# Optimization experiments

Hardware: AMD Instinct MI355X
Metric: run time of the kernel (lower is better)

The kernel has to match this reference:

```python
import jax, jax.numpy as jnp
import numpy as np

B, S, H = 2, 1024, 2048
NH, NKV, HD = 32, 8, 64
EPS = 1e-6
ROPE_BASE = 10000.0


def rms_norm(x, w, eps=EPS):
    xf = x.astype(jnp.float32)
    var = jnp.mean(xf * xf, axis=-1, keepdims=True)
    return (w * (xf * jax.lax.rsqrt(var + eps))).astype(x.dtype)


def rotate_half(x):
    x1, x2 = jnp.split(x, 2, axis=-1)
    return jnp.concatenate((-x2, x1), axis=-1)


def setup_inputs() -> dict:
    key = jax.random.key(0)
    ks = jax.random.split(key, 8)
    hidden_states = jax.random.normal(ks[0], (B, S, H), dtype=jnp.float32) * 0.02
    # real rotary embeddings for positions 0..S-1
    inv_freq = 1.0 / (ROPE_BASE ** (jnp.arange(0, HD, 2, dtype=jnp.float32) / HD))
    freqs = jnp.arange(S, dtype=jnp.float32)[:, None] * inv_freq[None, :]  # [S, HD/2]
    emb = jnp.concatenate((freqs, freqs), axis=-1)  # [S, HD]
    cos = jnp.broadcast_to(jnp.cos(emb)[None], (B, S, HD)).astype(jnp.float32)
    sin = jnp.broadcast_to(jnp.sin(emb)[None], (B, S, HD)).astype(jnp.float32)
    # additive causal mask [B, 1, S, S]
    causal = jnp.tril(jnp.ones((S, S), dtype=bool))
    attention_mask = jnp.broadcast_to(
        jnp.where(causal, 0.0, -1e9).astype(jnp.float32)[None, None], (B, 1, S, S))
    scale_in = 1.0 / np.sqrt(H)
    wq = jax.random.normal(ks[1], (H, NH * HD), dtype=jnp.float32) * scale_in
    wk = jax.random.normal(ks[2], (H, NKV * HD), dtype=jnp.float32) * scale_in
    wv = jax.random.normal(ks[3], (H, NKV * HD), dtype=jnp.float32) * scale_in
    wo = jax.random.normal(ks[4], (NH * HD, H), dtype=jnp.float32) * scale_in
    q_norm_w = jnp.ones((NH * HD,), dtype=jnp.float32)
    k_norm_w = jnp.ones((NKV * HD,), dtype=jnp.float32)
    return {"hidden_states": hidden_states, "cos": cos, "sin": sin,
            "attention_mask": attention_mask, "wq": wq, "wk": wk, "wv": wv,
            "wo": wo, "q_norm_w": q_norm_w, "k_norm_w": k_norm_w}


def reference(hidden_states, cos, sin, attention_mask, wq, wk, wv, wo, q_norm_w, k_norm_w):
    b, s, _ = hidden_states.shape
    scaling = HD ** -0.5
    groups = NH // NKV
    # projections + QK-norm (RMSNorm over full projected dim, before head split)
    q = rms_norm(hidden_states @ wq, q_norm_w)
    k = rms_norm(hidden_states @ wk, k_norm_w)
    v = hidden_states @ wv
    q = q.reshape(b, s, NH, HD).transpose(0, 2, 1, 3)   # [b, nh, s, hd]
    k = k.reshape(b, s, NKV, HD).transpose(0, 2, 1, 3)  # [b, nkv, s, hd]
    v = v.reshape(b, s, NKV, HD).transpose(0, 2, 1, 3)
    # RoPE (cos/sin broadcast over head dim)
    c = cos[:, None]  # [b, 1, s, hd]
    sn = sin[:, None]
    q = q * c + rotate_half(q) * sn
    k = k * c + rotate_half(k) * sn
    # GQA: repeat KV heads
    k = jnp.repeat(k, groups, axis=1)  # [b, nh, s, hd]
    v = jnp.repeat(v, groups, axis=1)
    scores = jnp.einsum('bhqd,bhkd->bhqk', q, k) * scaling + attention_mask
    attn = jax.nn.softmax(scores.astype(jnp.float32), axis=-1).astype(q.dtype)
    out = jnp.einsum('bhqk,bhkd->bhqd', attn, v)
    out = out.transpose(0, 2, 1, 3).reshape(b, s, NH * HD)
    return out @ wo
```

## Files before the change

### kernel.cpp

```cpp
#include <hip/hip_runtime.h>

#define B_    2
#define S_    1024
#define NH_   32
#define NKV_  8
#define T_    (B_*S_)

typedef unsigned short u16;
typedef unsigned int u32;
typedef __attribute__((ext_vector_type(8))) short bf16x8;
typedef __attribute__((ext_vector_type(4))) float f32x4;

__device__ __forceinline__ float bf2f(u16 u) {
    union { float f; unsigned int i; } c; c.i = ((unsigned int)u) << 16; return c.f;
}
__device__ __forceinline__ u16 f2bf(float f) {
    union { float f; unsigned int u; } c; c.f = f;
    return (u16)((c.u + 0x7FFFu + ((c.u >> 16) & 1u)) >> 16);
}

__device__ __forceinline__ void gld_lds16(const void* g, void* s) {
    __builtin_amdgcn_global_load_lds(
        (const __attribute__((address_space(1))) void*)g,
        (__attribute__((address_space(3))) void*)s,
        16, 0, 0);
}

__global__ __launch_bounds__(256) void preproc1(
    const float* __restrict__ hidden, const float* __restrict__ wq,
    const float* __restrict__ wk, const float* __restrict__ wv,
    const float* __restrict__ wo,
    u16* __restrict__ hidden_bf, u16* __restrict__ wqkvT, u16* __restrict__ woT)
{
    __shared__ float t[64][65];
    const int bid = blockIdx.x, tid = threadIdx.x;
    if (bid < 2048) {
        int i = (bid * 256 + tid) * 8;
        float4 v0 = *reinterpret_cast<const float4*>(&hidden[i]);
        float4 v1 = *reinterpret_cast<const float4*>(&hidden[i + 4]);
        u16 o[8] = { f2bf(v0.x), f2bf(v0.y), f2bf(v0.z), f2bf(v0.w),
                     f2bf(v1.x), f2bf(v1.y), f2bf(v1.z), f2bf(v1.w) };
        *reinterpret_cast<uint4*>(&hidden_bf[i]) = *reinterpret_cast<uint4*>(o);
        return;
    }
    const float* src; int scol, sN, n0, k0;
    u16* dst; int dK;
    if (bid < 3584) {
        const int tt = bid - 2048;
        n0 = (tt % 48) * 64; k0 = (tt / 48) * 64;
        if (n0 < 2048)      { src = wq; scol = n0;        sN = 2048; }
        else if (n0 < 2560) { src = wk; scol = n0 - 2048; sN = 512;  }
        else                { src = wv; scol = n0 - 2560; sN = 512;  }
        dst = wqkvT; dK = 2048;
    } else {
        const int tt = bid - 3584;
        n0 = (tt % 32) * 64; k0 = (tt / 32) * 64;
        src = wo; scol = n0; sN = 2048;
        dst = woT; dK = 2048;
    }
    #pragma unroll
    for (int i = 0; i < 16; ++i) {
        int e = i * 256 + tid, r = e >> 6, c = e & 63;
        t[r][c] = src[(size_t)(k0 + r) * sN + scol + c];
    }
    __syncthreads();
    #pragma unroll
    for (int i = 0; i < 16; ++i) {
        int e = i * 256 + tid, rr = e >> 6, cc = e & 63;
        dst[(size_t)(n0 + rr) * dK + k0 + cc] = f2bf(t[cc][rr]);
    }
}

template<bool OUT_BF16>
__global__ __launch_bounds__(256) void gemm_bt(
    const u16* __restrict__ A, const u16* __restrict__ Bt,
    void* __restrict__ Cv, int M, int N, int K)
{
    __shared__ u16 As[2][128 * 64];
    __shared__ u16 Bs[2][64 * 64];
    const int MB = M >> 7;
    const int cpx = gridDim.x >> 3;
    const int L = (blockIdx.x & 7) * cpx + (blockIdx.x >> 3);
    const int bm = (L % MB) * 128, bn = (L / MB) * 64;
    const int tid = threadIdx.x;
    const int w = tid >> 6, lane = tid & 63;
    const int wr = w >> 1, wc = w & 1;
    const int l15 = lane & 15, lg = lane >> 4;
    const int srow = lane >> 3;
    const int scolsw = (lane & 7) ^ srow;

    f32x4 acc[4][2] = {};
    const int nk = K >> 6;

#define GSTAGE(ks, bb) do {                                                    \
    const int kofs = (ks) * 64;                                                \
    _Pragma("unroll")                                                          \
    for (int i_ = 0; i_ < 4; ++i_) {                                           \
        int chunk_ = w * 4 + i_;                                               \
        int row_ = chunk_ * 8 + srow;                                          \
        gld_lds16(&A[(size_t)(bm + row_) * K + kofs + scolsw * 8],             \
                  &As[bb][chunk_ * 512]);                                      \
    }                                                                          \
    _Pragma("unroll")                                                          \
    for (int j_ = 0; j_ < 2; ++j_) {                                           \
        int chunk_ = w * 2 + j_;                                               \
        int row_ = chunk_ * 8 + srow;                                          \
        gld_lds16(&Bt[(size_t)(bn + row_) * K + kofs + scolsw * 8],            \
                  &Bs[bb][chunk_ * 512]);                                      \
    } } while (0)

    GSTAGE(0, 0);
    for (int ks = 0; ks < nk; ++ks) {
        const int cur = ks & 1;
        if (ks + 1 < nk) {
            GSTAGE(ks + 1, cur ^ 1);
            asm volatile("s_waitcnt vmcnt(6)" ::: "memory");
        } else {
            asm volatile("s_waitcnt vmcnt(0)" ::: "memory");
        }
        __builtin_amdgcn_sched_barrier(0);
        __builtin_amdgcn_s_barrier();
        __builtin_amdgcn_sched_barrier(0);

        #pragma unroll
        for (int kk = 0; kk < 2; ++kk) {
            const int phys = ((kk * 4 + lg) ^ (l15 & 7)) * 8;
            bf16x8 a[4], b[2];
            #pragma unroll
            for (int m = 0; m < 4; ++m)
                a[m] = *reinterpret_cast<const bf16x8*>(
                    &As[cur][(wr * 64 + m * 16 + l15) * 64 + phys]);
            #pragma unroll
            for (int n = 0; n < 2; ++n)
                b[n] = *reinterpret_cast<const bf16x8*>(
                    &Bs[cur][(wc * 32 + n * 16 + l15) * 64 + phys]);
            #pragma unroll
            for (int m = 0; m < 4; ++m)
                #pragma unroll
                for (int n = 0; n < 2; ++n)
                    acc[m][n] = __builtin_amdgcn_mfma_f32_16x16x32_bf16(
                        a[m], b[n], acc[m][n], 0, 0, 0);
        }
        __builtin_amdgcn_sched_barrier(0);
        __builtin_amdgcn_s_barrier();
    }
#undef GSTAGE

    const int orow0 = bm + wr * 64, ocol0 = bn + wc * 32;
    #pragma unroll
    for (int m = 0; m < 4; ++m)
        #pragma unroll
        for (int n = 0; n < 2; ++n)
            #pragma unroll
            for (int r = 0; r < 4; ++r) {
                int row = orow0 + m * 16 + lg * 4 + r;
                int col = ocol0 + n * 16 + l15;
                float v = acc[m][n][r];
                if (OUT_BF16)
                    ((u16*)Cv)[(size_t)row * N + col] = f2bf(v);
                else
                    ((float*)Cv)[(size_t)row * N + col] = v;
            }
}

template<int DIM>
__device__ __forceinline__ void rms_rope_row(
    u16* base, const float* __restrict__ w,
    const float* __restrict__ cs, const float* __restrict__ sn,
    float* row, float* red, int tid)
{
    float ss = 0.f;
    for (int i0 = tid * 8; i0 < DIM; i0 += 2048) {
        uint4 u = *reinterpret_cast<const uint4*>(&base[i0]);
        const u16* us = reinterpret_cast<const u16*>(&u);
        #pragma unroll
        for (int j = 0; j < 8; ++j) { float f = bf2f(us[j]); row[i0 + j] = f; ss += f * f; }
    }
    #pragma unroll
    for (int off = 1; off < 64; off <<= 1) ss += __shfl_xor(ss, off);
    if ((tid & 63) == 0) red[tid >> 6] = ss;
    __syncthreads();
    const float rstd = rsqrtf((red[0] + red[1] + red[2] + red[3]) * (1.0f / DIM) + 1e-6f);

    for (int i0 = tid * 8; i0 < DIM; i0 += 2048) {
        u16 o[8];
        #pragma unroll
        for (int j = 0; j < 8; ++j) {
            int i = i0 + j, dh = i & 63, bb = i & ~63;
            int oi = (dh < 32) ? bb + dh + 32 : bb + dh - 32;
            float y     = row[i]  * rstd * w[i];
            float other = row[oi] * rstd * w[oi];
            if (dh < 32) other = -other;
            o[j] = f2bf(y * cs[dh] + other * sn[dh]);
        }
        *reinterpret_cast<uint4*>(&base[i0]) = *reinterpret_cast<uint4*>(o);
    }
}

__global__ __launch_bounds__(256) void rmsnorm_rope_vt(
    u16* __restrict__ x, const float* __restrict__ qnw, const float* __restrict__ knw,
    const float* __restrict__ cosb, const float* __restrict__ sinb,
    u16* __restrict__ vT)
{
    __shared__ float smem[2304];
    const int bid = blockIdx.x, tid = threadIdx.x;
    if (bid < 2048) {
        const int t = bid;
        float* row = smem;
        float* red = smem + 2048;
        const float* cs = cosb + (size_t)t * 64;
        const float* sn = sinb + (size_t)t * 64;
        rms_rope_row<2048>(x + (size_t)t * 3072,        qnw, cs, sn, row, red, tid);
        __syncthreads();
        rms_rope_row<512 >(x + (size_t)t * 3072 + 2048, knw, cs, sn, row, red, tid);
        return;
    }
    u16 (*tu)[72] = reinterpret_cast<u16(*)[72]>(smem);
    const int bid2 = bid - 2048;
    const int hd = bid2 % 16;
    const int s0 = (bid2 / 16) * 64;
    const int b = hd >> 3, kvh = hd & 7;
    #pragma unroll
    for (int i = 0; i < 2; ++i) {
        int chunk = i * 256 + tid;
        int r = chunk >> 3, c8 = (chunk & 7) * 8;
        uint4 u = *reinterpret_cast<const uint4*>(
            &x[(size_t)(b * 1024 + s0 + r) * 3072 + 2560 + kvh * 64 + c8]);
        *reinterpret_cast<uint4*>(&tu[r][c8]) = u;
    }
    __syncthreads();
    #pragma unroll
    for (int i = 0; i < 2; ++i) {
        int chunk = i * 256 + tid;
        int d = chunk >> 3, c8 = (chunk & 7) * 8;
        u16 o[8];
        #pragma unroll
        for (int j = 0; j < 8; ++j) o[j] = tu[c8 + j][d];
        *reinterpret_cast<uint4*>(&vT[((size_t)(hd * 64 + d)) * 1024 + s0 + c8])
            = *reinterpret_cast<uint4*>(o);
    }
}

__global__ __launch_bounds__(256) void attn_pair(
    const u16* __restrict__ qkv,
    const u16* __restrict__ vT,
    u16* __restrict__ ob)
{
    __shared__ u16 Ks[2][64 * 64];
    __shared__ u16 Vs[2][64 * 64];
    __shared__ u16 Ps[4][16 * 64];

    const int bid = blockIdx.x;
    const int L   = (bid & 7) * 64 + (bid >> 3);
    const int g5  = L >> 5;
    const int rem = L & 31;
    const int ha  = rem & 3;
    const int p   = rem >> 2;
    const int b = g5 >> 3, kvh = g5 & 7;
    const int h = kvh * 4 + ha;
    const int qtA = p, qtB = 15 - p;

    const int tid = threadIdx.x, w = tid >> 6, lane = tid & 63;
    const int l15 = lane & 15, lg = lane >> 4;
    const int srow = lane >> 3;
    const int scolsw = (lane & 7) ^ srow;

    bf16x8 qfA[2], qfB[2];
    {
        const size_t rA = (size_t)(b * 1024 + qtA * 64 + w * 16 + l15);
        const size_t rB = (size_t)(b * 1024 + qtB * 64 + w * 16 + l15);
        #pragma unroll
        for (int kk = 0; kk < 2; ++kk) {
            qfA[kk] = *reinterpret_cast<const bf16x8*>(
                &qkv[rA * 3072 + h * 64 + kk * 32 + lg * 8]);
            qfB[kk] = *reinterpret_cast<const bf16x8*>(
                &qkv[rB * 3072 + h * 64 + kk * 32 + lg * 8]);
        }
    }
    asm volatile("s_waitcnt vmcnt(0)" ::: "memory");

    float lrA = 0.f, lrB = 0.f;
    f32x4 oaccA[4] = {}, oaccB[4] = {};

    const u16* kbase = qkv + 2048 + kvh * 64;
    const u16* vbase = vT + (size_t)(g5 * 64) * 1024;
    const int qgA = qtA * 64 + w * 16 + l15;
    const int qgB = qtB * 64 + w * 16 + l15;

#define ASTAGE(kt, bb) do {                                                    \
    _Pragma("unroll")                                                          \
    for (int i_ = 0; i_ < 2; ++i_) {                                           \
        int chunk_ = w * 2 + i_;                                               \
        int row_ = chunk_ * 8 + srow;                                          \
        gld_lds16(&kbase[(size_t)(b * 1024 + (kt) * 64 + row_) * 3072          \
                         + scolsw * 8], &Ks[bb][chunk_ * 512]);                \
        gld_lds16(&vbase[(size_t)row_ * 1024 + (kt) * 64 + scolsw * 8],        \
                  &Vs[bb][chunk_ * 512]);                                      \
    } } while (0)

    auto step = [&](int kt, int cur, const bf16x8 (&qf)[2],
                    float& lr, f32x4 (&oacc)[4], int qg, bool dz) {
        f32x4 sacc[4] = {};
        #pragma unroll
        for (int kk = 0; kk < 2; ++kk) {
            const int phys = ((kk * 4 + lg) ^ (l15 & 7)) * 8;
            #pragma unroll
            for (int m = 0; m < 4; ++m) {
                bf16x8 kf = *reinterpret_cast<const bf16x8*>(
                    &Ks[cur][(m * 16 + l15) * 64 + phys]);
                sacc[m] = __builtin_amdgcn_mfma_f32_16x16x32_bf16(
                    kf, qf[kk], sacc[m], 0, 0, 0);
            }
        }

        float ls = 0.f;
        #pragma unroll
        for (int m = 0; m < 4; ++m) {
            u16 pk[4];
            #pragma unroll
            for (int r = 0; r < 4; ++r) {
                float v = sacc[m][r] * 0.18033688f;
                if (dz && (kt * 64 + m * 16 + lg * 4 + r > qg)) v = -1e30f;
                float e = exp2f(v);
                ls += e;
                pk[r] = f2bf(e);
            }
            const int keyc = m * 16 + lg * 4;
            const int phys = (keyc >> 3) ^ (l15 & 7);
            *reinterpret_cast<uint2*>(&Ps[w][l15 * 64 + phys * 8 + (keyc & 7)])
                = *reinterpret_cast<const uint2*>(pk);
        }
        lr += ls;

        asm volatile("s_waitcnt lgkmcnt(0)" ::: "memory");
        __builtin_amdgcn_sched_barrier(0);

        #pragma unroll
        for (int kk = 0; kk < 2; ++kk) {
            const int phys = ((kk * 4 + lg) ^ (l15 & 7)) * 8;
            bf16x8 pf = *reinterpret_cast<const bf16x8*>(
                &Ps[w][l15 * 64 + phys]);
            #pragma unroll
            for (int d = 0; d < 4; ++d) {
                bf16x8 vf = *reinterpret_cast<const bf16x8*>(
                    &Vs[cur][(d * 16 + l15) * 64 + phys]);
                oacc[d] = __builtin_amdgcn_mfma_f32_16x16x32_bf16(
                    pf, vf, oacc[d], 0, 0, 0);
            }
        }
    };

    ASTAGE(0, 0);
    for (int s = 0; s <= 16; ++s) {
        const int cur = s & 1;
        if (s < 16) {
            const int ktn = (s + 1 <= p) ? (s + 1) : (s - p);
            ASTAGE(ktn, cur ^ 1);
            asm volatile("s_waitcnt vmcnt(4)" ::: "memory");
        } else {
            asm volatile("s_waitcnt vmcnt(0)" ::: "memory");
        }
        __builtin_amdgcn_sched_barrier(0);
        __builtin_amdgcn_s_barrier();
        __builtin_amdgcn_sched_barrier(0);

        if (s <= p) step(s,         cur, qfA, lrA, oaccA, qgA, s == p);
        else        step(s - p - 1, cur, qfB, lrB, oaccB, qgB, s == 16);

        __builtin_amdgcn_sched_barrier(0);
        __builtin_amdgcn_s_barrier();
    }
#undef ASTAGE

    #pragma unroll
    for (int tt = 0; tt < 2; ++tt) {
        const int qt = tt ? qtB : qtA;
        float lsum = tt ? lrB : lrA;
        lsum += __shfl_xor(lsum, 16);
        lsum += __shfl_xor(lsum, 32);
        f32x4* oacc = tt ? oaccB : oaccA;
        float linv[4];
        #pragma unroll
        for (int r = 0; r < 4; ++r) {
            float lv = __shfl(lsum, (lane & 48) + ((lane >> 4) & 3) * 4 + r);
            linv[r] = 1.f / lv;
        }
        #pragma unroll
        for (int d = 0; d < 4; ++d)
            #pragma unroll
            for (int r = 0; r < 4; ++r)
                ob[(size_t)(b * 1024 + qt * 64 + w * 16 + lg * 4 + r) * 2048
                   + h * 64 + d * 16 + l15] = f2bf(oacc[d][r] * linv[r]);
    }
}

extern "C" void kernel_launch(void* const* d_in, const int* in_sizes, int n_in,
                              void* d_out, int out_size, void* d_ws, size_t ws_size,
                              hipStream_t stream)
{
    const float* hidden = (const float*)d_in[0];
    const float* cosb   = (const float*)d_in[1];
    const float* sinb   = (const float*)d_in[2];
    const float* wq     = (const float*)d_in[4];
    const float* wk     = (const float*)d_in[5];
    const float* wv     = (const float*)d_in[6];
    const float* wo     = (const float*)d_in[7];
    const float* qnw    = (const float*)d_in[8];
    const float* knw    = (const float*)d_in[9];
    float* out = (float*)d_out;

    char* ws = (char*)d_ws;
    u16* hidden_bf = (u16*)ws;
    u16* wqkvT     = (u16*)(ws + ((size_t)8  << 20));
    u16* attn_bf   = (u16*)(ws + ((size_t)8  << 20));
    u16* qkv_bf    = (u16*)(ws + ((size_t)20 << 20));
    u16* v_bfT     = (u16*)(ws + ((size_t)32 << 20));
    u16* woT       = (u16*)(ws + ((size_t)34 << 20));

    preproc1<<<4608, 256, 0, stream>>>(hidden, wq, wk, wv, wo,
                                       hidden_bf, wqkvT, woT);

    gemm_bt<true><<<768, 256, 0, stream>>>(hidden_bf, wqkvT, qkv_bf,
                                           2048, 3072, 2048);

    rmsnorm_rope_vt<<<2304, 256, 0, stream>>>(qkv_bf, qnw, knw, cosb, sinb, v_bfT);

    attn_pair<<<512, 256, 0, stream>>>(qkv_bf, v_bfT, attn_bf);

    gemm_bt<false><<<512, 256, 0, stream>>>(attn_bf, woT, out,
                                            2048, 2048, 2048);
}
```

Measured before the change: 127.5 us.

## Switch attention to 32x32x16 MFMA with register-resident P and 2-wave blocks

Rewrites the attention kernel to use 32x32x16 bf16 MFMAs with two waves per block, each wave owning 32 query rows. Softmax probabilities are packed to bf16 with v_cvt_pk_bf16_f32 and rearranged into the PV operand through cross-half-wave shuffles, so the LDS P buffer round-trip is gone. This cuts LDS traffic and per-row reduction shuffles, but halves threads per block, which raises per-thread load work and accumulator register pressure.

```diff
diff --git a/kernel.cpp b/kernel.cpp
--- a/kernel.cpp
+++ b/kernel.cpp
@@ -10,6 +10,7 @@
 typedef unsigned int u32;
 typedef __attribute__((ext_vector_type(8))) short bf16x8;
 typedef __attribute__((ext_vector_type(4))) float f32x4;
+typedef __attribute__((ext_vector_type(16))) float f32x16;
 
 __device__ __forceinline__ float bf2f(u16 u) {
     union { float f; unsigned int i; } c; c.i = ((unsigned int)u) << 16; return c.f;
@@ -17,6 +18,11 @@
 __device__ __forceinline__ u16 f2bf(float f) {
     union { float f; unsigned int u; } c; c.f = f;
     return (u16)((c.u + 0x7FFFu + ((c.u >> 16) & 1u)) >> 16);
+}
+__device__ __forceinline__ u32 cvtpk(float lo, float hi) {
+    u32 r;
+    asm("v_cvt_pk_bf16_f32 %0, %1, %2" : "=v"(r) : "v"(lo), "v"(hi));
+    return r;
 }
 
 __device__ __forceinline__ void gld_lds16(const void* g, void* s) {
@@ -241,14 +247,13 @@
     }
 }
 
-__global__ __launch_bounds__(256) void attn_pair(
+__global__ __launch_bounds__(128) void attn_pair32(
     const u16* __restrict__ qkv,
     const u16* __restrict__ vT,
     u16* __restrict__ ob)
 {
     __shared__ u16 Ks[2][64 * 64];
     __shared__ u16 Vs[2][64 * 64];
-    __shared__ u16 Ps[4][16 * 64];
 
     const int bid = blockIdx.x;
     const int L   = (bid & 7) * 64 + (bid >> 3);
@@ -258,39 +263,39 @@
     const int p   = rem >> 2;
     const int b = g5 >> 3, kvh = g5 & 7;
     const int h = kvh * 4 + ha;
-    const int qtA = p, qtB = 15 - p;
+    const int spA = p, spB = 15 - p;
+    const int tilesA = p + 1;
 
     const int tid = threadIdx.x, w = tid >> 6, lane = tid & 63;
-    const int l15 = lane & 15, lg = lane >> 4;
+    const int l31 = lane & 31, hi = lane >> 5;
     const int srow = lane >> 3;
     const int scolsw = (lane & 7) ^ srow;
 
-    bf16x8 qfA[2], qfB[2];
+    const int qA_seq = spA * 64 + w * 32 + l31;
+    const int qB_seq = spB * 64 + w * 32 + l31;
+
+    bf16x8 qfA[4], qfB[4];
     {
-        const size_t rA = (size_t)(b * 1024 + qtA * 64 + w * 16 + l15);
-        const size_t rB = (size_t)(b * 1024 + qtB * 64 + w * 16 + l15);
-        #pragma unroll
-        for (int kk = 0; kk < 2; ++kk) {
-            qfA[kk] = *reinterpret_cast<const bf16x8*>(
-                &qkv[rA * 3072 + h * 64 + kk * 32 + lg * 8]);
-            qfB[kk] = *reinterpret_cast<const bf16x8*>(
-                &qkv[rB * 3072 + h * 64 + kk * 32 + lg * 8]);
+        const u16* qra = qkv + (size_t)(b * 1024 + qA_seq) * 3072 + h * 64;
+        const u16* qrb = qkv + (size_t)(b * 1024 + qB_seq) * 3072 + h * 64;
+        #pragma unroll
+        for (int s = 0; s < 4; ++s) {
+            qfA[s] = *reinterpret_cast<const bf16x8*>(&qra[s * 16 + hi * 8]);
+            qfB[s] = *reinterpret_cast<const bf16x8*>(&qrb[s * 16 + hi * 8]);
         }
     }
     asm volatile("s_waitcnt vmcnt(0)" ::: "memory");
 
     float lrA = 0.f, lrB = 0.f;
-    f32x4 oaccA[4] = {}, oaccB[4] = {};
+    f32x16 oaccA[2] = {}, oaccB[2] = {};
 
     const u16* kbase = qkv + 2048 + kvh * 64;
     const u16* vbase = vT + (size_t)(g5 * 64) * 1024;
-    const int qgA = qtA * 64 + w * 16 + l15;
-    const int qgB = qtB * 64 + w * 16 + l15;
 
 #define ASTAGE(kt, bb) do {                                                    \
     _Pragma("unroll")                                                          \
-    for (int i_ = 0; i_ < 2; ++i_) {                                           \
-        int chunk_ = w * 2 + i_;                                               \
+    for (int i_ = 0; i_ < 4; ++i_) {                                           \
+        int chunk_ = w * 4 + i_;                                               \
         int row_ = chunk_ * 8 + srow;                                          \
         gld_lds16(&kbase[(size_t)(b * 1024 + (kt) * 64 + row_) * 3072          \
                          + scolsw * 8], &Ks[bb][chunk_ * 512]);                \
@@ -298,65 +303,77 @@
                   &Vs[bb][chunk_ * 512]);                                      \
     } } while (0)
 
-    auto step = [&](int kt, int cur, const bf16x8 (&qf)[2],
-                    float& lr, f32x4 (&oacc)[4], int qg, bool dz) {
-        f32x4 sacc[4] = {};
-        #pragma unroll
-        for (int kk = 0; kk < 2; ++kk) {
-            const int phys = ((kk * 4 + lg) ^ (l15 & 7)) * 8;
-            #pragma unroll
-            for (int m = 0; m < 4; ++m) {
+    auto step = [&](int kt, int cur, const bf16x8 (&qf)[4],
+                    float& lr, f32x16 (&oacc)[2], int q_seq, bool dz) {
+        f32x16 sacc[2] = {};
+        #pragma unroll
+        for (int gg = 0; gg < 2; ++gg)
+            #pragma unroll
+            for (int s = 0; s < 4; ++s) {
+                const int phys = ((s * 2 + hi) ^ (l31 & 7)) * 8;
                 bf16x8 kf = *reinterpret_cast<const bf16x8*>(
-                    &Ks[cur][(m * 16 + l15) * 64 + phys]);
-                sacc[m] = __builtin_amdgcn_mfma_f32_16x16x32_bf16(
-                    kf, qf[kk], sacc[m], 0, 0, 0);
-            }
-        }
-
-        float ls = 0.f;
-        #pragma unroll
-        for (int m = 0; m < 4; ++m) {
-            u16 pk[4];
-            #pragma unroll
-            for (int r = 0; r < 4; ++r) {
-                float v = sacc[m][r] * 0.18033688f;
-                if (dz && (kt * 64 + m * 16 + lg * 4 + r > qg)) v = -1e30f;
+                    &Ks[cur][(gg * 32 + l31) * 64 + phys]);
+                sacc[gg] = __builtin_amdgcn_mfma_f32_32x32x16_bf16(
+                    kf, qf[s], sacc[gg], 0, 0, 0);
+            }
+
+        const float SC = 0.18033688f;
+        float pv[2][16];
+        #pragma unroll
+        for (int gg = 0; gg < 2; ++gg)
+            #pragma unroll
+            for (int r = 0; r < 16; ++r) {
+                float v = sacc[gg][r] * SC;
+                if (dz) {
+                    const int key = kt * 64 + gg * 32
+                                  + (r & 3) + 8 * (r >> 2) + 4 * hi;
+                    if (key > q_seq) v = -1e30f;
+                }
                 float e = exp2f(v);
-                ls += e;
-                pk[r] = f2bf(e);
-            }
-            const int keyc = m * 16 + lg * 4;
-            const int phys = (keyc >> 3) ^ (l15 & 7);
-            *reinterpret_cast<uint2*>(&Ps[w][l15 * 64 + phys * 8 + (keyc & 7)])
-                = *reinterpret_cast<const uint2*>(pk);
-        }
-        lr += ls;
-
-        asm volatile("s_waitcnt lgkmcnt(0)" ::: "memory");
-        __builtin_amdgcn_sched_barrier(0);
-
-        #pragma unroll
-        for (int kk = 0; kk < 2; ++kk) {
-            const int phys = ((kk * 4 + lg) ^ (l15 & 7)) * 8;
-            bf16x8 pf = *reinterpret_cast<const bf16x8*>(
-                &Ps[w][l15 * 64 + phys]);
-            #pragma unroll
-            for (int d = 0; d < 4; ++d) {
+                pv[gg][r] = e;
+                lr += e;
+            }
+
+        bf16x8 pfrag[4];
+        #pragma unroll
+        for (int gg = 0; gg < 2; ++gg)
+            #pragma unroll
+            for (int hh = 0; hh < 2; ++hh) {
+                const int r0 = hh * 8;
+                u32 Aw = cvtpk(pv[gg][r0+0], pv[gg][r0+1]);
+                u32 Bw = cvtpk(pv[gg][r0+2], pv[gg][r0+3]);
+                u32 Cw = cvtpk(pv[gg][r0+4], pv[gg][r0+5]);
+                u32 Dw = cvtpk(pv[gg][r0+6], pv[gg][r0+7]);
+                u32 Ax = __shfl_xor(Aw, 32), Bx = __shfl_xor(Bw, 32);
+                u32 Cx = __shfl_xor(Cw, 32), Dx = __shfl_xor(Dw, 32);
+                u32 ww[4];
+                ww[0] = hi ? Cx : Aw;
+                ww[1] = hi ? Dx : Bw;
+                ww[2] = hi ? Cw : Ax;
+                ww[3] = hi ? Dw : Bx;
+                pfrag[gg * 2 + hh] = *reinterpret_cast<const bf16x8*>(ww);
+            }
+
+        #pragma unroll
+        for (int dg = 0; dg < 2; ++dg)
+            #pragma unroll
+            for (int s = 0; s < 4; ++s) {
+                const int phys = ((s * 2 + hi) ^ (l31 & 7)) * 8;
                 bf16x8 vf = *reinterpret_cast<const bf16x8*>(
-                    &Vs[cur][(d * 16 + l15) * 64 + phys]);
-                oacc[d] = __builtin_amdgcn_mfma_f32_16x16x32_bf16(
-                    pf, vf, oacc[d], 0, 0, 0);
-            }
-        }
+                    &Vs[cur][(dg * 32 + l31) * 64 + phys]);
+                oacc[dg] = __builtin_amdgcn_mfma_f32_32x32x16_bf16(
+                    vf, pfrag[s], oacc[dg], 0, 0, 0);
+            }
     };
 
     ASTAGE(0, 0);
     for (int s = 0; s <= 16; ++s) {
         const int cur = s & 1;
         if (s < 16) {
-            const int ktn = (s + 1 <= p) ? (s + 1) : (s - p);
+            const int sn = s + 1;
+            const int ktn = (sn < tilesA) ? sn : (sn - tilesA);
             ASTAGE(ktn, cur ^ 1);
-            asm volatile("s_waitcnt vmcnt(4)" ::: "memory");
+            asm volatile("s_waitcnt vmcnt(8)" ::: "memory");
         } else {
             asm volatile("s_waitcnt vmcnt(0)" ::: "memory");
         }
@@ -364,8 +381,10 @@
         __builtin_amdgcn_s_barrier();
         __builtin_amdgcn_sched_barrier(0);
 
-        if (s <= p) step(s,         cur, qfA, lrA, oaccA, qgA, s == p);
-        else        step(s - p - 1, cur, qfB, lrB, oaccB, qgB, s == 16);
+        if (s < tilesA)
+            step(s,          cur, qfA, lrA, oaccA, qA_seq, s == tilesA - 1);
+        else
+            step(s - tilesA, cur, qfB, lrB, oaccB, qB_seq, s == 16);
 
         __builtin_amdgcn_sched_barrier(0);
         __builtin_amdgcn_s_barrier();
@@ -374,23 +393,23 @@
 
     #pragma unroll
     for (int tt = 0; tt < 2; ++tt) {
-        const int qt = tt ? qtB : qtA;
-        float lsum = tt ? lrB : lrA;
-        lsum += __shfl_xor(lsum, 16);
-        lsum += __shfl_xor(lsum, 32);
-        f32x4* oacc = tt ? oaccB : oaccA;
-        float linv[4];
-        #pragma unroll
-        for (int r = 0; r < 4; ++r) {
-            float lv = __shfl(lsum, (lane & 48) + ((lane >> 4) & 3) * 4 + r);
-            linv[r] = 1.f / lv;
-        }
-        #pragma unroll
-        for (int d = 0; d < 4; ++d)
-            #pragma unroll
-            for (int r = 0; r < 4; ++r)
-                ob[(size_t)(b * 1024 + qt * 64 + w * 16 + lg * 4 + r) * 2048
-                   + h * 64 + d * 16 + l15] = f2bf(oacc[d][r] * linv[r]);
+        const int q_seq = tt ? qB_seq : qA_seq;
+        float lr = tt ? lrB : lrA;
+        const float lsum = lr + __shfl_xor(lr, 32);
+        const float linv = 1.f / lsum;
+        f32x16* oacc = tt ? oaccB : oaccA;
+        u16* orow = ob + (size_t)(b * 1024 + q_seq) * 2048 + h * 64;
+        #pragma unroll
+        for (int dg = 0; dg < 2; ++dg)
+            #pragma unroll
+            for (int rq = 0; rq < 4; ++rq) {
+                u16 o4[4];
+                #pragma unroll
+                for (int j = 0; j < 4; ++j)
+                    o4[j] = f2bf(oacc[dg][rq * 4 + j] * linv);
+                *reinterpret_cast<uint2*>(&orow[dg * 32 + 8 * rq + 4 * hi])
+                    = *reinterpret_cast<const uint2*>(o4);
+            }
     }
 }
 
@@ -425,7 +444,7 @@
 
     rmsnorm_rope_vt<<<2304, 256, 0, stream>>>(qkv_bf, qnw, knw, cosb, sinb, v_bfT);
 
-    attn_pair<<<512, 256, 0, stream>>>(qkv_bf, v_bfT, attn_bf);
+    attn_pair32<<<512, 128, 0, stream>>>(qkv_bf, v_bfT, attn_bf);
 
     gemm_bt<false><<<512, 256, 0, stream>>>(attn_bf, woT, out,
                                             2048, 2048, 2048);
```

After: 144.5 us, median of 2. 13.3% more time.

## Software-pipeline attention: overlap PV of previous tile with QK softmax of current

Applied to the files above, without the earlier changes.

Splits the per-tile attention step into a QK+softmax phase and a PV phase. The PV for tile t-1 now runs in the same iteration as QK/softmax for tile t. V is triple-buffered and P double-buffered per wave so the lagged PV reads stay valid. The goal is to hide the LDS wait between writing P and reading it back, and to interleave MFMA with exp work. In exchange it uses more LDS, which may lower occupancy, and adds an extra loop iteration.

```diff
diff --git a/kernel.cpp b/kernel.cpp
--- a/kernel.cpp
+++ b/kernel.cpp
@@ -241,14 +241,14 @@
     }
 }
 
-__global__ __launch_bounds__(256) void attn_pair(
+__global__ __launch_bounds__(256) void attn_pipe(
     const u16* __restrict__ qkv,
     const u16* __restrict__ vT,
     u16* __restrict__ ob)
 {
     __shared__ u16 Ks[2][64 * 64];
-    __shared__ u16 Vs[2][64 * 64];
-    __shared__ u16 Ps[4][16 * 64];
+    __shared__ u16 Vs[3][64 * 64];
+    __shared__ u16 Ps[4][2][16 * 64];
 
     const int bid = blockIdx.x;
     const int L   = (bid & 7) * 64 + (bid >> 3);
@@ -259,6 +259,7 @@
     const int b = g5 >> 3, kvh = g5 & 7;
     const int h = kvh * 4 + ha;
     const int qtA = p, qtB = 15 - p;
+    const int tilesA = p + 1;
 
     const int tid = threadIdx.x, w = tid >> 6, lane = tid & 63;
     const int l15 = lane & 15, lg = lane >> 4;
@@ -287,19 +288,19 @@
     const int qgA = qtA * 64 + w * 16 + l15;
     const int qgB = qtB * 64 + w * 16 + l15;
 
-#define ASTAGE(kt, bb) do {                                                    \
+#define ASTAGE(kt, kb, vb) do {                                                \
     _Pragma("unroll")                                                          \
     for (int i_ = 0; i_ < 2; ++i_) {                                           \
         int chunk_ = w * 2 + i_;                                               \
         int row_ = chunk_ * 8 + srow;                                          \
         gld_lds16(&kbase[(size_t)(b * 1024 + (kt) * 64 + row_) * 3072          \
-                         + scolsw * 8], &Ks[bb][chunk_ * 512]);                \
+                         + scolsw * 8], &Ks[kb][chunk_ * 512]);                \
         gld_lds16(&vbase[(size_t)row_ * 1024 + (kt) * 64 + scolsw * 8],        \
-                  &Vs[bb][chunk_ * 512]);                                      \
+                  &Vs[vb][chunk_ * 512]);                                      \
     } } while (0)
 
-    auto step = [&](int kt, int cur, const bf16x8 (&qf)[2],
-                    float& lr, f32x4 (&oacc)[4], int qg, bool dz) {
+    auto qksm = [&](int kt, int kcur, int par, const bf16x8 (&qf)[2],
+                    float& lr, int qg, bool dz) {
         f32x4 sacc[4] = {};
         #pragma unroll
         for (int kk = 0; kk < 2; ++kk) {
@@ -307,12 +308,11 @@
             #pragma unroll
             for (int m = 0; m < 4; ++m) {
                 bf16x8 kf = *reinterpret_cast<const bf16x8*>(
-                    &Ks[cur][(m * 16 + l15) * 64 + phys]);
+                    &Ks[kcur][(m * 16 + l15) * 64 + phys]);
                 sacc[m] = __builtin_amdgcn_mfma_f32_16x16x32_bf16(
                     kf, qf[kk], sacc[m], 0, 0, 0);
             }
         }
-
         float ls = 0.f;
         #pragma unroll
         for (int m = 0; m < 4; ++m) {
@@ -327,45 +327,56 @@
             }
             const int keyc = m * 16 + lg * 4;
             const int phys = (keyc >> 3) ^ (l15 & 7);
-            *reinterpret_cast<uint2*>(&Ps[w][l15 * 64 + phys * 8 + (keyc & 7)])
+            *reinterpret_cast<uint2*>(
+                &Ps[w][par][l15 * 64 + phys * 8 + (keyc & 7)])
                 = *reinterpret_cast<const uint2*>(pk);
         }
         lr += ls;
-
-        asm volatile("s_waitcnt lgkmcnt(0)" ::: "memory");
-        __builtin_amdgcn_sched_barrier(0);
-
+    };
+
+    auto pv = [&](int par, int vidx, f32x4 (&oacc)[4]) {
         #pragma unroll
         for (int kk = 0; kk < 2; ++kk) {
             const int phys = ((kk * 4 + lg) ^ (l15 & 7)) * 8;
             bf16x8 pf = *reinterpret_cast<const bf16x8*>(
-                &Ps[w][l15 * 64 + phys]);
+                &Ps[w][par][l15 * 64 + phys]);
             #pragma unroll
             for (int d = 0; d < 4; ++d) {
                 bf16x8 vf = *reinterpret_cast<const bf16x8*>(
-                    &Vs[cur][(d * 16 + l15) * 64 + phys]);
+                    &Vs[vidx][(d * 16 + l15) * 64 + phys]);
                 oacc[d] = __builtin_amdgcn_mfma_f32_16x16x32_bf16(
                     pf, vf, oacc[d], 0, 0, 0);
             }
         }
     };
 
-    ASTAGE(0, 0);
-    for (int s = 0; s <= 16; ++s) {
-        const int cur = s & 1;
-        if (s < 16) {
-            const int ktn = (s + 1 <= p) ? (s + 1) : (s - p);
-            ASTAGE(ktn, cur ^ 1);
-            asm volatile("s_waitcnt vmcnt(4)" ::: "memory");
-        } else {
-            asm volatile("s_waitcnt vmcnt(0)" ::: "memory");
-        }
-        __builtin_amdgcn_sched_barrier(0);
-        __builtin_amdgcn_s_barrier();
-        __builtin_amdgcn_sched_barrier(0);
-
-        if (s <= p) step(s,         cur, qfA, lrA, oaccA, qgA, s == p);
-        else        step(s - p - 1, cur, qfB, lrB, oaccB, qgB, s == 16);
+    ASTAGE(0, 0, 0);
+    for (int s = 0; s <= 17; ++s) {
+        if (s <= 16) {
+            if (s < 16) {
+                const int sn = s + 1;
+                const int ktn = (sn < tilesA) ? sn : (sn - tilesA);
+                ASTAGE(ktn, sn & 1, sn % 3);
+                asm volatile("s_waitcnt vmcnt(4)" ::: "memory");
+            } else {
+                asm volatile("s_waitcnt vmcnt(0)" ::: "memory");
+            }
+            __builtin_amdgcn_sched_barrier(0);
+            __builtin_amdgcn_s_barrier();
+            __builtin_amdgcn_sched_barrier(0);
+        }
+
+        if (s >= 1) {
+            const int t = s - 1;
+            if (t < tilesA) pv(t & 1, t % 3, oaccA);
+            else            pv(t & 1, t % 3, oaccB);
+        }
+        if (s <= 16) {
+            if (s < tilesA)
+                qksm(s, s & 1, s & 1, qfA, lrA, qgA, s == tilesA - 1);
+            else
+                qksm(s - tilesA, s & 1, s & 1, qfB, lrB, qgB, s == 16);
+        }
 
         __builtin_amdgcn_sched_barrier(0);
         __builtin_amdgcn_s_barrier();
@@ -425,7 +436,7 @@
 
     rmsnorm_rope_vt<<<2304, 256, 0, stream>>>(qkv_bf, qnw, knw, cosb, sinb, v_bfT);
 
-    attn_pair<<<512, 256, 0, stream>>>(qkv_bf, v_bfT, attn_bf);
+    attn_pipe<<<512, 256, 0, stream>>>(qkv_bf, v_bfT, attn_bf);
 
     gemm_bt<false><<<512, 256, 0, stream>>>(attn_bf, woT, out,
                                             2048, 2048, 2048);
```

New measurement: 130.4 us. 2.3% more time.

## Use 128-key KV tiles in paired causal attention kernel

Applied to the files above, without the earlier changes.

Doubles the key/value tile in the attention kernel from 64 to 128 keys, halving the number of pipeline steps and barriers per block and giving more MFMAs per LDS stage. The swizzles for V and P are redone for the wider rows, and s_setprio is raised around the MFMA sections. In exchange LDS use doubles, which may reduce occupancy. Causal masking now does more wasted work on diagonal tiles because each tile holds 128 keys while a query tile is 64 rows.

```diff
diff --git a/kernel.cpp b/kernel.cpp
--- a/kernel.cpp
+++ b/kernel.cpp
@@ -241,14 +241,14 @@
     }
 }
 
-__global__ __launch_bounds__(256) void attn_pair(
+__global__ __launch_bounds__(256) void attn_128(
     const u16* __restrict__ qkv,
     const u16* __restrict__ vT,
     u16* __restrict__ ob)
 {
-    __shared__ u16 Ks[2][64 * 64];
-    __shared__ u16 Vs[2][64 * 64];
-    __shared__ u16 Ps[4][16 * 64];
+    __shared__ u16 Ks[2][128 * 64];
+    __shared__ u16 Vs[2][64 * 128];
+    __shared__ u16 Ps[4][16 * 128];
 
     const int bid = blockIdx.x;
     const int L   = (bid & 7) * 64 + (bid >> 3);
@@ -259,6 +259,7 @@
     const int b = g5 >> 3, kvh = g5 & 7;
     const int h = kvh * 4 + ha;
     const int qtA = p, qtB = 15 - p;
+    const int tilesA = (p >> 1) + 1;
 
     const int tid = threadIdx.x, w = tid >> 6, lane = tid & 63;
     const int l15 = lane & 15, lg = lane >> 4;
@@ -289,45 +290,49 @@
 
 #define ASTAGE(kt, bb) do {                                                    \
     _Pragma("unroll")                                                          \
-    for (int i_ = 0; i_ < 2; ++i_) {                                           \
-        int chunk_ = w * 2 + i_;                                               \
-        int row_ = chunk_ * 8 + srow;                                          \
-        gld_lds16(&kbase[(size_t)(b * 1024 + (kt) * 64 + row_) * 3072          \
+    for (int i_ = 0; i_ < 4; ++i_) {                                           \
+        int chunk_ = w * 4 + i_;                                               \
+        int krow_ = chunk_ * 8 + srow;                                         \
+        gld_lds16(&kbase[(size_t)(b * 1024 + (kt) * 128 + krow_) * 3072        \
                          + scolsw * 8], &Ks[bb][chunk_ * 512]);                \
-        gld_lds16(&vbase[(size_t)row_ * 1024 + (kt) * 64 + scolsw * 8],        \
+        int vrow_ = chunk_ * 4 + (lane >> 4);                                  \
+        int vcol_ = (lane & 15) ^ (vrow_ & 15);                                \
+        gld_lds16(&vbase[(size_t)vrow_ * 1024 + (kt) * 128 + vcol_ * 8],       \
                   &Vs[bb][chunk_ * 512]);                                      \
     } } while (0)
 
     auto step = [&](int kt, int cur, const bf16x8 (&qf)[2],
                     float& lr, f32x4 (&oacc)[4], int qg, bool dz) {
-        f32x4 sacc[4] = {};
+        f32x4 sacc[8] = {};
+        __builtin_amdgcn_s_setprio(1);
         #pragma unroll
         for (int kk = 0; kk < 2; ++kk) {
             const int phys = ((kk * 4 + lg) ^ (l15 & 7)) * 8;
             #pragma unroll
-            for (int m = 0; m < 4; ++m) {
+            for (int m = 0; m < 8; ++m) {
                 bf16x8 kf = *reinterpret_cast<const bf16x8*>(
                     &Ks[cur][(m * 16 + l15) * 64 + phys]);
                 sacc[m] = __builtin_amdgcn_mfma_f32_16x16x32_bf16(
                     kf, qf[kk], sacc[m], 0, 0, 0);
             }
         }
+        __builtin_amdgcn_s_setprio(0);
 
         float ls = 0.f;
         #pragma unroll
-        for (int m = 0; m < 4; ++m) {
+        for (int m = 0; m < 8; ++m) {
             u16 pk[4];
             #pragma unroll
             for (int r = 0; r < 4; ++r) {
                 float v = sacc[m][r] * 0.18033688f;
-                if (dz && (kt * 64 + m * 16 + lg * 4 + r > qg)) v = -1e30f;
+                if (dz && (kt * 128 + m * 16 + lg * 4 + r > qg)) v = -1e30f;
                 float e = exp2f(v);
                 ls += e;
                 pk[r] = f2bf(e);
             }
-            const int keyc = m * 16 + lg * 4;
-            const int phys = (keyc >> 3) ^ (l15 & 7);
-            *reinterpret_cast<uint2*>(&Ps[w][l15 * 64 + phys * 8 + (keyc & 7)])
+            const int cl = ((m * 2 + (lg >> 1)) ^ l15);
+            *reinterpret_cast<uint2*>(
+                &Ps[w][l15 * 128 + cl * 8 + (lg & 1) * 4])
                 = *reinterpret_cast<const uint2*>(pk);
         }
         lr += ls;
@@ -335,28 +340,31 @@
         asm volatile("s_waitcnt lgkmcnt(0)" ::: "memory");
         __builtin_amdgcn_sched_barrier(0);
 
-        #pragma unroll
-        for (int kk = 0; kk < 2; ++kk) {
-            const int phys = ((kk * 4 + lg) ^ (l15 & 7)) * 8;
+        __builtin_amdgcn_s_setprio(1);
+        #pragma unroll
+        for (int kk = 0; kk < 4; ++kk) {
+            const int c = (kk * 4 + lg) ^ l15;
             bf16x8 pf = *reinterpret_cast<const bf16x8*>(
-                &Ps[w][l15 * 64 + phys]);
+                &Ps[w][l15 * 128 + c * 8]);
             #pragma unroll
             for (int d = 0; d < 4; ++d) {
                 bf16x8 vf = *reinterpret_cast<const bf16x8*>(
-                    &Vs[cur][(d * 16 + l15) * 64 + phys]);
+                    &Vs[cur][(d * 16 + l15) * 128 + c * 8]);
                 oacc[d] = __builtin_amdgcn_mfma_f32_16x16x32_bf16(
                     pf, vf, oacc[d], 0, 0, 0);
             }
         }
+        __builtin_amdgcn_s_setprio(0);
     };
 
     ASTAGE(0, 0);
-    for (int s = 0; s <= 16; ++s) {
+    for (int s = 0; s < 9; ++s) {
         const int cur = s & 1;
-        if (s < 16) {
-            const int ktn = (s + 1 <= p) ? (s + 1) : (s - p);
+        if (s < 8) {
+            const int sn = s + 1;
+            const int ktn = (sn < tilesA) ? sn : (sn - tilesA);
             ASTAGE(ktn, cur ^ 1);
-            asm volatile("s_waitcnt vmcnt(4)" ::: "memory");
+            asm volatile("s_waitcnt vmcnt(8)" ::: "memory");
         } else {
             asm volatile("s_waitcnt vmcnt(0)" ::: "memory");
         }
@@ -364,8 +372,10 @@
         __builtin_amdgcn_s_barrier();
         __builtin_amdgcn_sched_barrier(0);
 
-        if (s <= p) step(s,         cur, qfA, lrA, oaccA, qgA, s == p);
-        else        step(s - p - 1, cur, qfB, lrB, oaccB, qgB, s == 16);
+        if (s < tilesA)
+            step(s,          cur, qfA, lrA, oaccA, qgA, s == tilesA - 1);
+        else
+            step(s - tilesA, cur, qfB, lrB, oaccB, qgB, s == 8);
 
         __builtin_amdgcn_sched_barrier(0);
         __builtin_amdgcn_s_barrier();
@@ -425,7 +435,7 @@
 
     rmsnorm_rope_vt<<<2304, 256, 0, stream>>>(qkv_bf, qnw, knw, cosb, sinb, v_bfT);
 
-    attn_pair<<<512, 256, 0, stream>>>(qkv_bf, v_bfT, attn_bf);
+    attn_128<<<512, 256, 0, stream>>>(qkv_bf, v_bfT, attn_bf);
 
     gemm_bt<false><<<512, 256, 0, stream>>>(attn_bf, woT, out,
                                             2048, 2048, 2048);
```

After: 129.3 us. No clear change (+1.4%).
